# Kernel optimization log

Hardware: AMD Instinct MI355X
Metric: run time of the kernel (lower is better)

## Reference

```python
import jax, jax.numpy as jnp
import numpy as np

B, VH, VL, EP = 4, 130, 120, 256
DIN, DEP, D, H, NL = 256, 128, 512, 16, 8
HID = 4 * D

def _pe(x, base=1000.0):
    # sinusoidal positional encoding (base=1000 as in the module)
    L, Dm = x.shape[-2], x.shape[-1]
    pos = jnp.arange(L, dtype=jnp.float32)
    ch = jnp.arange(Dm, dtype=jnp.float32)
    ang = pos[:, None] / (base ** (2.0 * ch / ch[-1]))[None]
    enc = jnp.where(ch % 2 == 0, jnp.sin(ang), jnp.cos(ang))
    return x + enc

def _ln(x, g, b):
    m = x.mean(-1, keepdims=True)
    v = ((x - m) ** 2).mean(-1, keepdims=True)
    return (x - m) / jnp.sqrt(v + 1e-5) * g + b

def _gmha(x, rots, trans, mask_bias, qkv_w, out_w, out_b, g, b, r_s, d_s):
    # ESM3 geometric multi-head attention (algorithm 6)
    xn = _ln(x, g, b)
    qkv = (xn @ qkv_w.T).reshape(x.shape[0], x.shape[1], 5, H, 3)  # [B,L,5,H,3]
    qkv = jnp.einsum('brid,brfhd->brfhi', rots, qkv)               # rotate into global frame
    Qr, Kr, Qd, Kd, V = (qkv[..., f, :, :] for f in range(5))
    scale = 3.0 ** -0.5
    Ar = jnp.einsum('bihd,bjhd->bijh', Qr, Kr) * jax.nn.softplus(r_s) * scale
    qd = Qd + trans[:, :, None, :]
    kd = Kd + trans[:, :, None, :]
    dist = jnp.linalg.norm(qd[:, :, None] - kd[:, None], axis=-1)  # [B,i,j,H]
    logits = Ar - dist * jax.nn.softplus(d_s) * scale + mask_bias[..., None]
    A = jax.nn.softmax(logits, axis=2)
    o = jnp.einsum('bijh,bjhd->bihd', A, V)
    o = jnp.einsum('brji,brhj->brhi', rots, o)                     # rotate back (R^T)
    return o.reshape(x.shape[0], x.shape[1], H * 3) @ out_w.T + out_b

def _swiglu(x, g, b, w12, w3):
    # SwiGLU transition (dropout is identity in eval)
    h = _ln(x, g, b) @ w12.T
    a, v = jnp.split(h, 2, axis=-1)
    return (jax.nn.silu(a) * v) @ w3.T

def _forward(vh_x, vl_x, vh_rots, vh_trans, vl_rots, vl_trans, ep_feats, ep_rots, ep_trans,
             vh_emb_w, vl_emb_w, tgt_emb_w, qkv_w, out_w, out_b, ln_g, ln_b, r_scale, d_scale,
             ln2_g, ln2_b, w12, w3, out_vh_w, out_vh_gate_w, out_vh_gate_b,
             out_vl_w, out_vl_gate_w, out_vl_gate_b, vh_mask, vl_mask, ep_mask):
    emb = jnp.concatenate([_pe(vh_x @ vh_emb_w.T), _pe(vl_x @ vl_emb_w.T), ep_feats @ tgt_emb_w.T], axis=1)
    rots = jnp.concatenate([vh_rots, vl_rots, ep_rots], axis=1)
    trans = jnp.concatenate([vh_trans, vl_trans, ep_trans], axis=1)
    mask = jnp.concatenate([vh_mask, vl_mask, ep_mask], axis=1)
    mask_bias = jnp.where(mask[:, :, None] | mask[:, None, :], -1e9, 0.0)
    for i in range(NL):
        emb = emb + _gmha(emb, rots, trans, mask_bias, qkv_w[i], out_w[i], out_b[i],
                          ln_g[i], ln_b[i], r_scale[i], d_scale[i])
        emb = emb + _swiglu(emb, ln2_g[i], ln2_b[i], w12[i], w3[i])
    vh_e, vl_e = emb[:, :VH], emb[:, VH:VH + VL]
    vh_upd = (vh_e @ out_vh_w.T) * jax.nn.sigmoid(vh_e @ out_vh_gate_w.T + out_vh_gate_b)
    vl_upd = (vl_e @ out_vl_w.T) * jax.nn.sigmoid(vl_e @ out_vl_gate_w.T + out_vl_gate_b)
    vh_out = jnp.where(~vh_mask[..., None], vh_x + vh_upd, vh_x)
    vl_out = jnp.where(~vl_mask[..., None], vl_x + vl_upd, vl_x)
    return vh_out, vl_out

def setup_inputs():
    key = jax.random.key(0)
    ks = iter(jax.random.split(key, 40))
    s = 0.02
    return dict(
        vh_x=jax.random.normal(next(ks), (B, VH, DIN)),
        vl_x=jax.random.normal(next(ks), (B, VL, DIN)),
        vh_rots=jax.random.normal(next(ks), (B, VH, 3, 3)),
        vh_trans=jax.random.normal(next(ks), (B, VH, 3)),
        vl_rots=jax.random.normal(next(ks), (B, VL, 3, 3)),
        vl_trans=jax.random.normal(next(ks), (B, VL, 3)),
        ep_feats=jax.random.normal(next(ks), (B, EP, DEP)),
        ep_rots=jax.random.normal(next(ks), (B, EP, 3, 3)),
        ep_trans=jax.random.normal(next(ks), (B, EP, 3)),
        vh_mask=jnp.zeros((B, VH), dtype=bool),
        vl_mask=jnp.zeros((B, VL), dtype=bool),
        ep_mask=jax.random.randint(next(ks), (B, EP), 0, 2).astype(bool),
        vh_emb_w=jax.random.normal(next(ks), (D, DIN)) * s,
        vl_emb_w=jax.random.normal(next(ks), (D, DIN)) * s,
        tgt_emb_w=jax.random.normal(next(ks), (D, DEP)) * s,
        qkv_w=jax.random.normal(next(ks), (NL, H * 15, D)) * s,
        out_w=jax.random.normal(next(ks), (NL, D, H * 3)) * s,
        out_b=jnp.zeros((NL, D)),
        ln_g=jnp.ones((NL, D)), ln_b=jnp.zeros((NL, D)),
        r_scale=jnp.zeros((NL, H)), d_scale=jnp.zeros((NL, H)),
        ln2_g=jnp.ones((NL, D)), ln2_b=jnp.zeros((NL, D)),
        w12=jax.random.normal(next(ks), (NL, 2 * HID, D)) * s,
        w3=jax.random.normal(next(ks), (NL, D, HID)) * s,
        out_vh_w=jax.random.normal(next(ks), (DIN, D)) * s,
        out_vh_gate_w=jax.random.normal(next(ks), (DIN, D)) * s,
        out_vh_gate_b=jnp.full((DIN,), -2.0),
        out_vl_w=jax.random.normal(next(ks), (DIN, D)) * s,
        out_vl_gate_w=jax.random.normal(next(ks), (DIN, D)) * s,
        out_vl_gate_b=jnp.full((DIN,), -2.0),
    )

def reference(vh_x, vl_x, vh_rots, vh_trans, vl_rots, vl_trans, ep_feats, ep_rots, ep_trans,
              vh_mask, vl_mask, ep_mask,
              vh_emb_w, vl_emb_w, tgt_emb_w, qkv_w, out_w, out_b, ln_g, ln_b, r_scale, d_scale,
              ln2_g, ln2_b, w12, w3, out_vh_w, out_vh_gate_w, out_vh_gate_b,
              out_vl_w, out_vl_gate_w, out_vl_gate_b):
    return _forward(vh_x, vl_x, vh_rots, vh_trans, vl_rots, vl_trans, ep_feats, ep_rots, ep_trans,
                    vh_emb_w, vl_emb_w, tgt_emb_w, qkv_w, out_w, out_b, ln_g, ln_b, r_scale, d_scale,
                    ln2_g, ln2_b, w12, w3, out_vh_w, out_vh_gate_w, out_vh_gate_b,
                    out_vl_w, out_vl_gate_w, out_vl_gate_b, vh_mask, vl_mask, ep_mask)
```

## Files before the change

### kernel.cpp

```cpp
#include <hip/hip_runtime.h>
#include <hip/hip_bf16.h>
#include <math.h>
#include <stdint.h>

#define B_ 4
#define VH_ 130
#define VL_ 120
#define EP_ 256
#define R_ 506
#define RP_ 512
#define DIN_ 256
#define DEP_ 128
#define D_ 512
#define H_ 16
#define NL_ 8
#define HID_ 2048

#define MODE_STORE 0
#define MODE_ADD_BIAS 1

typedef _Float16 half8 __attribute__((ext_vector_type(8)));
typedef float f32x4 __attribute__((ext_vector_type(4)));

#define ASYNC16(ldsdst, gsrc)                                                  \
  __builtin_amdgcn_global_load_lds(                                            \
      (const __attribute__((address_space(1))) unsigned int*)(gsrc),           \
      (__attribute__((address_space(3))) unsigned int*)(ldsdst), 16, 0, 0)

__global__ __launch_bounds__(256) void gemm16sw_kernel(
    const _Float16* __restrict__ A, const _Float16* __restrict__ Wa,
    const _Float16* __restrict__ Wv, _Float16* __restrict__ Gh,
    int M, int K) {
  __shared__ _Float16 Al[4][4096];
  __shared__ _Float16 Ba[4][2048];
  __shared__ _Float16 Bv[4][2048];

  const int t = threadIdx.x;
  const int nbm = (M + 127) >> 7;
  const int nwg = gridDim.x;
  int bid = blockIdx.x;
  if ((nwg & 7) == 0) {
    int q = nwg >> 3;
    bid = (bid & 7) * q + (bid >> 3);
  }
  const int bm = bid % nbm, bn = bid / nbm;
  const int lane = t & 63;
  const int w = t >> 6;
  const int wm = w >> 1, wn = w & 1;

  const int r0 = t >> 2;
  const int cp = t & 3;
  const int gc = cp ^ ((r0 >> 1) & 3);
  int gr0 = bm * 128 + r0;       if (gr0 >= M) gr0 = M - 1;
  int gr1 = bm * 128 + 64 + r0;  if (gr1 >= M) gr1 = M - 1;
  const int gcol = bn * 64 + r0;
  const _Float16* pA0 = A + (size_t)gr0 * K + gc * 8;
  const _Float16* pA1 = A + (size_t)gr1 * K + gc * 8;
  const _Float16* pBa = Wa + (size_t)gcol * K + gc * 8;
  const _Float16* pBv = Wv + (size_t)gcol * K + gc * 8;

#define STAGE(buf, kt)                                                         \
  do {                                                                         \
    ASYNC16(&Al[buf][t * 8], pA0 + (size_t)(kt) * 32);                         \
    ASYNC16(&Al[buf][2048 + t * 8], pA1 + (size_t)(kt) * 32);                  \
    ASYNC16(&Ba[buf][t * 8], pBa + (size_t)(kt) * 32);                         \
    ASYNC16(&Bv[buf][t * 8], pBv + (size_t)(kt) * 32);                         \
  } while (0)

  f32x4 aca[4][2], acv[4][2];
#pragma unroll
  for (int i = 0; i < 4; i++)
#pragma unroll
    for (int j = 0; j < 2; j++) {
      aca[i][j] = (f32x4){0.f, 0.f, 0.f, 0.f};
      acv[i][j] = (f32x4){0.f, 0.f, 0.f, 0.f};
    }

  const int nt = K >> 5;
  STAGE(0, 0); STAGE(1, 1); STAGE(2, 2);

  const int rl = lane & 15;
  const int ca = (lane >> 4) ^ ((rl >> 1) & 3);
  for (int kt = 0; kt < nt; ++kt) {
    if (kt < nt - 2)       asm volatile("s_waitcnt vmcnt(8)" ::: "memory");
    else if (kt == nt - 2) asm volatile("s_waitcnt vmcnt(4)" ::: "memory");
    else                   asm volatile("s_waitcnt vmcnt(0)" ::: "memory");
    __builtin_amdgcn_s_barrier();
    const int buf = kt & 3;
    const _Float16* Ab  = &Al[buf][(wm * 64 + rl) * 32 + ca * 8];
    const _Float16* Bab = &Ba[buf][(wn * 32 + rl) * 32 + ca * 8];
    const _Float16* Bvb = &Bv[buf][(wn * 32 + rl) * 32 + ca * 8];
    half8 af[4], bfa[2], bfv[2];
#pragma unroll
    for (int i = 0; i < 4; i++) af[i] = *(const half8*)(Ab + i * 512);
#pragma unroll
    for (int j = 0; j < 2; j++) {
      bfa[j] = *(const half8*)(Bab + j * 512);
      bfv[j] = *(const half8*)(Bvb + j * 512);
    }
#pragma unroll
    for (int i = 0; i < 4; i++)
#pragma unroll
      for (int j = 0; j < 2; j++) {
        aca[i][j] = __builtin_amdgcn_mfma_f32_16x16x32_f16(af[i], bfa[j],
                                                           aca[i][j], 0, 0, 0);
        acv[i][j] = __builtin_amdgcn_mfma_f32_16x16x32_f16(af[i], bfv[j],
                                                           acv[i][j], 0, 0, 0);
      }
    if (kt + 3 < nt) STAGE((kt + 3) & 3, kt + 3);
  }
#undef STAGE

  const int rb = bm * 128 + wm * 64 + ((lane >> 4) << 2);
  const int cb = bn * 64 + wn * 32 + (lane & 15);
#pragma unroll
  for (int i = 0; i < 4; i++) {
#pragma unroll
    for (int j = 0; j < 2; j++) {
      int col = cb + j * 16;
#pragma unroll
      for (int q = 0; q < 4; q++) {
        int row = rb + i * 16 + q;
        if (row >= M) continue;
        float a = aca[i][j][q];
        float v = acv[i][j][q];
        Gh[(size_t)row * HID_ + col] = (_Float16)((a / (1.f + expf(-a))) * v);
      }
    }
  }
}

__global__ __launch_bounds__(256) void gemm16b_kernel(
    const _Float16* __restrict__ A, const _Float16* __restrict__ W,
    float* __restrict__ C, const float* __restrict__ bias,
    int M, int N, int K, int mode, int crpb, int cR, int cbase, int pe) {
  __shared__ _Float16 Al[4][2048];
  __shared__ _Float16 Bl[4][2048];

  const int t = threadIdx.x;
  const int nbm = (M + 63) >> 6;
  const int nwg = gridDim.x;
  int bid = blockIdx.x;
  if ((nwg & 7) == 0) {
    int q = nwg >> 3;
    bid = (bid & 7) * q + (bid >> 3);
  }
  const int bm = bid % nbm, bn = bid / nbm;
  const int lane = t & 63;
  const int w = t >> 6;
  const int wm = w >> 1, wn = w & 1;

  const int r0 = t >> 2;
  const int cp = t & 3;
  const int gc = cp ^ ((r0 >> 1) & 3);
  int gr = bm * 64 + r0;    if (gr >= M) gr = M - 1;
  int gcol = bn * 64 + r0;  if (gcol >= N) gcol = N - 1;
  const _Float16* pA = A + (size_t)gr * K + gc * 8;
  const _Float16* pB = W + (size_t)gcol * K + gc * 8;

#define STAGE(buf, kt)                                                         \
  do {                                                                         \
    ASYNC16(&Al[buf][t * 8], pA + (size_t)(kt) * 32);                          \
    ASYNC16(&Bl[buf][t * 8], pB + (size_t)(kt) * 32);                          \
  } while (0)

  f32x4 acc[2][2];
#pragma unroll
  for (int i = 0; i < 2; i++)
#pragma unroll
    for (int j = 0; j < 2; j++) acc[i][j] = (f32x4){0.f, 0.f, 0.f, 0.f};

  const int nt = K >> 5;
  STAGE(0, 0); STAGE(1, 1); STAGE(2, 2);

  const int rl = lane & 15;
  const int ca = (lane >> 4) ^ ((rl >> 1) & 3);
  for (int kt = 0; kt < nt; ++kt) {
    if (kt < nt - 2)       asm volatile("s_waitcnt vmcnt(4)" ::: "memory");
    else if (kt == nt - 2) asm volatile("s_waitcnt vmcnt(2)" ::: "memory");
    else                   asm volatile("s_waitcnt vmcnt(0)" ::: "memory");
    __builtin_amdgcn_s_barrier();
    const int buf = kt & 3;
    half8 af[2], bf[2];
#pragma unroll
    for (int i = 0; i < 2; i++)
      af[i] = *(const half8*)&Al[buf][(wm * 32 + i * 16 + rl) * 32 + ca * 8];
#pragma unroll
    for (int j = 0; j < 2; j++)
      bf[j] = *(const half8*)&Bl[buf][(wn * 32 + j * 16 + rl) * 32 + ca * 8];
#pragma unroll
    for (int i = 0; i < 2; i++)
#pragma unroll
      for (int j = 0; j < 2; j++)
        acc[i][j] = __builtin_amdgcn_mfma_f32_16x16x32_f16(af[i], bf[j],
                                                           acc[i][j], 0, 0, 0);
    if (kt + 3 < nt) STAGE((kt + 3) & 3, kt + 3);
  }
#undef STAGE

  const float PEK = -0.02703623196464017f;
  const int rb = bm * 64 + wm * 32 + ((lane >> 4) << 2);
  const int cb = bn * 64 + wn * 32 + (lane & 15);
#pragma unroll
  for (int i = 0; i < 2; i++) {
#pragma unroll
    for (int j = 0; j < 2; j++) {
      int col = cb + j * 16;
      if (col >= N) continue;
#pragma unroll
      for (int q = 0; q < 4; q++) {
        int row = rb + i * 16 + q;
        if (row >= M) continue;
        int crow = (row / crpb) * cR + cbase + row % crpb;
        size_t idx = (size_t)crow * N + col;
        float v = acc[i][j][q];
        if (pe) {
          float pos = (float)(row % crpb);
          float ang = pos * expf((float)col * PEK);
          v += (col & 1) ? cosf(ang) : sinf(ang);
        }
        if (mode == MODE_STORE) C[idx] = v;
        else {
          float bb = bias ? bias[col] : 0.f;
          C[idx] = C[idx] + v + bb;
        }
      }
    }
  }
}

__global__ __launch_bounds__(256) void gemm16gate_kernel(
    const _Float16* __restrict__ A, const _Float16* __restrict__ Wv,
    const _Float16* __restrict__ Wg, const float* __restrict__ x,
    const float* __restrict__ gb, const int* __restrict__ mask,
    float* __restrict__ out, int M, int K, int arpb, int aR, int abase) {
  __shared__ _Float16 Al[4][2048];
  __shared__ _Float16 Bva[4][2048];
  __shared__ _Float16 Bga[4][2048];

  const int t = threadIdx.x;
  const int nbm = (M + 63) >> 6;
  const int nwg = gridDim.x;
  int bid = blockIdx.x;
  if ((nwg & 7) == 0) {
    int q = nwg >> 3;
    bid = (bid & 7) * q + (bid >> 3);
  }
  const int bm = bid % nbm, bn = bid / nbm;
  const int lane = t & 63;
  const int w = t >> 6;
  const int wm = w >> 1, wn = w & 1;

  const int r0 = t >> 2;
  const int cp = t & 3;
  const int gc = cp ^ ((r0 >> 1) & 3);
  int gr = bm * 64 + r0;  if (gr >= M) gr = M - 1;
  int ar = (gr / arpb) * aR + abase + gr % arpb;
  const int gcol = bn * 64 + r0;
  const _Float16* pA  = A + (size_t)ar * K + gc * 8;
  const _Float16* pBv = Wv + (size_t)gcol * K + gc * 8;
  const _Float16* pBg = Wg + (size_t)gcol * K + gc * 8;

#define STAGE(buf, kt)                                                         \
  do {                                                                         \
    ASYNC16(&Al[buf][t * 8], pA + (size_t)(kt) * 32);                          \
    ASYNC16(&Bva[buf][t * 8], pBv + (size_t)(kt) * 32);                        \
    ASYNC16(&Bga[buf][t * 8], pBg + (size_t)(kt) * 32);                        \
  } while (0)

  f32x4 acv[2][2], acg[2][2];
#pragma unroll
  for (int i = 0; i < 2; i++)
#pragma unroll
    for (int j = 0; j < 2; j++) {
      acv[i][j] = (f32x4){0.f, 0.f, 0.f, 0.f};
      acg[i][j] = (f32x4){0.f, 0.f, 0.f, 0.f};
    }

  const int nt = K >> 5;
  STAGE(0, 0); STAGE(1, 1); STAGE(2, 2);

  const int rl = lane & 15;
  const int ca = (lane >> 4) ^ ((rl >> 1) & 3);
  for (int kt = 0; kt < nt; ++kt) {
    if (kt < nt - 2)       asm volatile("s_waitcnt vmcnt(6)" ::: "memory");
    else if (kt == nt - 2) asm volatile("s_waitcnt vmcnt(3)" ::: "memory");
    else                   asm volatile("s_waitcnt vmcnt(0)" ::: "memory");
    __builtin_amdgcn_s_barrier();
    const int buf = kt & 3;
    half8 af[2], bv[2], bg2[2];
#pragma unroll
    for (int i = 0; i < 2; i++)
      af[i] = *(const half8*)&Al[buf][(wm * 32 + i * 16 + rl) * 32 + ca * 8];
#pragma unroll
    for (int j = 0; j < 2; j++) {
      bv[j] = *(const half8*)&Bva[buf][(wn * 32 + j * 16 + rl) * 32 + ca * 8];
      bg2[j] = *(const half8*)&Bga[buf][(wn * 32 + j * 16 + rl) * 32 + ca * 8];
    }
#pragma unroll
    for (int i = 0; i < 2; i++)
#pragma unroll
      for (int j = 0; j < 2; j++) {
        acv[i][j] = __builtin_amdgcn_mfma_f32_16x16x32_f16(af[i], bv[j],
                                                           acv[i][j], 0, 0, 0);
        acg[i][j] = __builtin_amdgcn_mfma_f32_16x16x32_f16(af[i], bg2[j],
                                                           acg[i][j], 0, 0, 0);
      }
    if (kt + 3 < nt) STAGE((kt + 3) & 3, kt + 3);
  }
#undef STAGE

  const int rb = bm * 64 + wm * 32 + ((lane >> 4) << 2);
  const int cb = bn * 64 + wn * 32 + (lane & 15);
#pragma unroll
  for (int i = 0; i < 2; i++) {
#pragma unroll
    for (int j = 0; j < 2; j++) {
      int col = cb + j * 16;
#pragma unroll
      for (int q = 0; q < 4; q++) {
        int row = rb + i * 16 + q;
        if (row >= M) continue;
        size_t idx = (size_t)row * DIN_ + col;
        float xv = x[idx];
        float res;
        if (mask[row]) {
          res = xv;
        } else {
          float gate = 1.f / (1.f + expf(-(acg[i][j][q] + gb[col])));
          res = xv + acv[i][j][q] * gate;
        }
        out[idx] = res;
      }
    }
  }
}

__global__ __launch_bounds__(256) void ln_kernel(
    const float* __restrict__ x, const float* __restrict__ g,
    const float* __restrict__ b, _Float16* __restrict__ out) {
  const int row = blockIdx.x;
  const int t = threadIdx.x;
  const float* xr = x + (size_t)row * D_;
  float v0 = xr[t], v1 = xr[t + 256];
  float s = v0 + v1, s2 = v0 * v0 + v1 * v1;
#pragma unroll
  for (int o = 32; o > 0; o >>= 1) {
    s += __shfl_down(s, o);
    s2 += __shfl_down(s2, o);
  }
  __shared__ float w1[4], w2[4], mv[2];
  const int w = t >> 6;
  if ((t & 63) == 0) { w1[w] = s; w2[w] = s2; }
  __syncthreads();
  if (t == 0) {
    float ss = w1[0] + w1[1] + w1[2] + w1[3];
    float ss2 = w2[0] + w2[1] + w2[2] + w2[3];
    float mean = ss * (1.f / D_);
    float var = ss2 * (1.f / D_) - mean * mean;
    mv[0] = mean;
    mv[1] = rsqrtf(var + 1e-5f);
  }
  __syncthreads();
  float mean = mv[0], inv = mv[1];
  _Float16* orow = out + (size_t)row * D_;
  orow[t] = (_Float16)((v0 - mean) * inv * g[t] + b[t]);
  orow[t + 256] = (_Float16)((v1 - mean) * inv * g[t + 256] + b[t + 256]);
}

struct ThSegs {
  const float* src[13];
  _Float16* dst[13];
  int cum[14];
};
__global__ void tohalf_multi_kernel(ThSegs sg) {
  int total = sg.cum[13];
  for (int i = blockIdx.x * blockDim.x + threadIdx.x; i < total;
       i += gridDim.x * blockDim.x) {
    int s = 0;
    while (i >= sg.cum[s + 1]) s++;
    int off = i - sg.cum[s];
    const float4* p = (const float4*)(sg.src[s] + (size_t)off * 16);
    float4 x = p[0], y = p[1], z = p[2], w = p[3];
    half8 h0 = {(_Float16)x.x, (_Float16)x.y, (_Float16)x.z, (_Float16)x.w,
                (_Float16)y.x, (_Float16)y.y, (_Float16)y.z, (_Float16)y.w};
    half8 h1 = {(_Float16)z.x, (_Float16)z.y, (_Float16)z.z, (_Float16)z.w,
                (_Float16)w.x, (_Float16)w.y, (_Float16)w.z, (_Float16)w.w};
    half8* d = (half8*)(sg.dst[s] + (size_t)off * 16);
    d[0] = h0;
    d[1] = h1;
  }
}

__global__ void tohalf_kernel(const float* __restrict__ src,
                              _Float16* __restrict__ dst, int n8) {
  for (int i = blockIdx.x * blockDim.x + threadIdx.x; i < n8;
       i += gridDim.x * blockDim.x) {
    const float4* s = (const float4*)(src + (size_t)i * 8);
    float4 x = s[0], y = s[1];
    half8 h = {(_Float16)x.x, (_Float16)x.y, (_Float16)x.z, (_Float16)x.w,
               (_Float16)y.x, (_Float16)y.y, (_Float16)y.z, (_Float16)y.w};
    *(half8*)(dst + (size_t)i * 8) = h;
  }
}

__global__ void transpose_ow_kernel(const float* __restrict__ out_w,
                                    float* __restrict__ owT) {
  int idx = blockIdx.x * blockDim.x + threadIdx.x;
  const int total = NL_ * 48 * D_;
  if (idx >= total) return;
  int l = idx / (48 * D_);
  int rem = idx % (48 * D_);
  int k = rem / D_;
  int c = rem % D_;
  owT[idx] = out_w[(size_t)l * D_ * 48 + (size_t)c * 48 + k];
}

__global__ void prep_kernel(
    const float* __restrict__ vh_rots, const float* __restrict__ vh_trans,
    const float* __restrict__ vl_rots, const float* __restrict__ vl_trans,
    const float* __restrict__ ep_rots, const float* __restrict__ ep_trans,
    const int* __restrict__ vh_mask, const int* __restrict__ vl_mask,
    const int* __restrict__ ep_mask, float* __restrict__ rots,
    float* __restrict__ trans, int* __restrict__ mask,
    int* __restrict__ maskp, float* __restrict__ Kt, float* __restrict__ PKt,
    float* __restrict__ Vt) {
  int idx = blockIdx.x * blockDim.x + threadIdx.x;
  if (idx < B_ * RP_) {
    int b = idx >> 9, r = idx & (RP_ - 1);
    if (r >= R_) {
      maskp[idx] = 1;
      return;
    }
    const float* sr; const float* st; int sm;
    if (r < VH_) {
      sr = vh_rots + (size_t)(b * VH_ + r) * 9;
      st = vh_trans + (size_t)(b * VH_ + r) * 3;
      sm = vh_mask[b * VH_ + r];
    } else if (r < VH_ + VL_) {
      int rr = r - VH_;
      sr = vl_rots + (size_t)(b * VL_ + rr) * 9;
      st = vl_trans + (size_t)(b * VL_ + rr) * 3;
      sm = vl_mask[b * VL_ + rr];
    } else {
      int rr = r - VH_ - VL_;
      sr = ep_rots + (size_t)(b * EP_ + rr) * 9;
      st = ep_trans + (size_t)(b * EP_ + rr) * 3;
      sm = ep_mask[b * EP_ + rr];
    }
    int lin = b * R_ + r;
    maskp[idx] = sm;
    mask[lin] = sm;
#pragma unroll
    for (int k = 0; k < 9; k++) rots[(size_t)lin * 9 + k] = sr[k];
#pragma unroll
    for (int k = 0; k < 3; k++) trans[(size_t)lin * 3 + k] = st[k];
  } else {
    int p = idx - B_ * RP_;
    const int per = B_ * H_ * 3 * (RP_ - R_);
    if (p >= 3 * per) return;
    int a = p / per;
    int q = p % per;
    int chan = q / (RP_ - R_), jj = q % (RP_ - R_);
    float* dst = (a == 0) ? Kt : (a == 1) ? PKt : Vt;
    dst[(size_t)chan * RP_ + R_ + jj] = 0.f;
  }
}

__global__ __launch_bounds__(128) void rotate_kernel(
    const float* __restrict__ qkv_raw, const float* __restrict__ rots,
    const float* __restrict__ trans, float* __restrict__ Qrow,
    float* __restrict__ PQrow, float* __restrict__ Kt,
    float* __restrict__ PKt, float* __restrict__ Vt) {
  const int blk = blockIdx.x;
  const int b = blk / R_;
  const int r = blk % R_;
  const int t = threadIdx.x;
  __shared__ float Rm[9], tr[3], raw[240];
  if (t < 9) Rm[t] = rots[(size_t)blk * 9 + t];
  if (t >= 9 && t < 12) tr[t - 9] = trans[(size_t)blk * 3 + (t - 9)];
  for (int i = t; i < 240; i += 128) raw[i] = qkv_raw[(size_t)blk * 240 + i];
  __syncthreads();
  if (t < 80) {
    int f = t / 16, h = t % 16;
    float x = raw[f * 48 + h * 3 + 0];
    float y = raw[f * 48 + h * 3 + 1];
    float z = raw[f * 48 + h * 3 + 2];
    float r0 = Rm[0] * x + Rm[1] * y + Rm[2] * z;
    float r1 = Rm[3] * x + Rm[4] * y + Rm[5] * z;
    float r2 = Rm[6] * x + Rm[7] * y + Rm[8] * z;
    if (f == 2 || f == 3) { r0 += tr[0]; r1 += tr[1]; r2 += tr[2]; }
    if (f == 0 || f == 2) {
      float* dst = (f == 0) ? Qrow : PQrow;
      size_t o = (size_t)blk * 48 + h * 3;
      dst[o] = r0; dst[o + 1] = r1; dst[o + 2] = r2;
    } else {
      float* dst = (f == 1) ? Kt : (f == 3) ? PKt : Vt;
      size_t base = ((size_t)(b * H_ + h) * 3) * RP_ + r;
      dst[base] = r0; dst[base + RP_] = r1; dst[base + 2 * RP_] = r2;
    }
  }
}

__global__ __launch_bounds__(1024) void attn2_kernel(
    const float* __restrict__ Qrow, const float* __restrict__ PQrow,
    const float* __restrict__ Kt, const float* __restrict__ PKt,
    const float* __restrict__ Vt, const float* __restrict__ rots,
    const int* __restrict__ mask, const int* __restrict__ maskp,
    const float* __restrict__ rs, const float* __restrict__ ds,
    const float* __restrict__ owT, const float* __restrict__ out_b,
    float* __restrict__ emb) {
  const int blk = blockIdx.x;
  const int b = blk / (R_ / 2);
  const int ip = blk % (R_ / 2);
  const int i0 = ip * 2;
  const int t = threadIdx.x;
  const int lane = t & 63;
  const int h = t >> 6;

  __shared__ float qs[2][48], ps[2][48], og[2][48];
  __shared__ float crs[16], cds[16];
  __shared__ int mi[2];

  if (t < 96) {
    int io = t / 48, k2 = t % 48;
    int i = i0 + io;
    qs[io][k2] = Qrow[((size_t)(b * R_ + i)) * 48 + k2];
    ps[io][k2] = PQrow[((size_t)(b * R_ + i)) * 48 + k2];
  } else if (t < 112) {
    int hh = t - 96;
    const float sc = 0.57735026918962576f;
    crs[hh] = log1pf(expf(rs[hh])) * sc;
    cds[hh] = log1pf(expf(ds[hh])) * sc;
  } else if (t < 114) {
    mi[t - 112] = mask[b * R_ + i0 + (t - 112)];
  }
  __syncthreads();

  float mb[8];
#pragma unroll
  for (int jb = 0; jb < 8; jb++) {
    int j = jb * 64 + lane;
    mb[jb] = maskp[b * RP_ + j] ? -1e9f : 0.f;
  }
  const float bi0 = mi[0] ? -1e9f : 0.f;
  const float bi1 = mi[1] ? -1e9f : 0.f;

  {
    const float sA = crs[h], sD = cds[h];
    const float qx0 = qs[0][h * 3], qy0 = qs[0][h * 3 + 1], qz0 = qs[0][h * 3 + 2];
    const float px0 = ps[0][h * 3], py0 = ps[0][h * 3 + 1], pz0 = ps[0][h * 3 + 2];
    const float qx1 = qs[1][h * 3], qy1 = qs[1][h * 3 + 1], qz1 = qs[1][h * 3 + 2];
    const float px1 = ps[1][h * 3], py1 = ps[1][h * 3 + 1], pz1 = ps[1][h * 3 + 2];
    const float* kb = Kt + ((size_t)(b * H_ + h) * 3) * RP_;
    const float* pb = PKt + ((size_t)(b * H_ + h) * 3) * RP_;
    const float* vb = Vt + ((size_t)(b * H_ + h) * 3) * RP_;

    float l0[8], l1[8];
    float m0 = -3e38f, m1 = -3e38f;
#pragma unroll
    for (int jb = 0; jb < 8; jb++) {
      int j = jb * 64 + lane;
      float kx = kb[j], ky = kb[j + RP_], kz = kb[j + 2 * RP_];
      float pkx = pb[j], pky = pb[j + RP_], pkz = pb[j + 2 * RP_];
      float dx0 = px0 - pkx, dy0 = py0 - pky, dz0 = pz0 - pkz;
      float d0 = sqrtf(dx0 * dx0 + dy0 * dy0 + dz0 * dz0);
      l0[jb] = (qx0 * kx + qy0 * ky + qz0 * kz) * sA - d0 * sD + mb[jb] + bi0;
      m0 = fmaxf(m0, l0[jb]);
      float dx1 = px1 - pkx, dy1 = py1 - pky, dz1 = pz1 - pkz;
      float d1 = sqrtf(dx1 * dx1 + dy1 * dy1 + dz1 * dz1);
      l1[jb] = (qx1 * kx + qy1 * ky + qz1 * kz) * sA - d1 * sD + mb[jb] + bi1;
      m1 = fmaxf(m1, l1[jb]);
    }
#pragma unroll
    for (int s = 1; s < 64; s <<= 1) {
      m0 = fmaxf(m0, __shfl_xor(m0, s));
      m1 = fmaxf(m1, __shfl_xor(m1, s));
    }
    float s0 = 0.f, s1 = 0.f;
    float ox0 = 0.f, oy0 = 0.f, oz0 = 0.f, ox1 = 0.f, oy1 = 0.f, oz1 = 0.f;
#pragma unroll
    for (int jb = 0; jb < 8; jb++) {
      int j = jb * 64 + lane;
      float p0 = expf(l0[jb] - m0);
      float p1 = expf(l1[jb] - m1);
      s0 += p0; s1 += p1;
      float vx = vb[j], vy = vb[j + RP_], vz = vb[j + 2 * RP_];
      ox0 += p0 * vx; oy0 += p0 * vy; oz0 += p0 * vz;
      ox1 += p1 * vx; oy1 += p1 * vy; oz1 += p1 * vz;
    }
#pragma unroll
    for (int s = 1; s < 64; s <<= 1) {
      s0 += __shfl_xor(s0, s); s1 += __shfl_xor(s1, s);
      ox0 += __shfl_xor(ox0, s); oy0 += __shfl_xor(oy0, s); oz0 += __shfl_xor(oz0, s);
      ox1 += __shfl_xor(ox1, s); oy1 += __shfl_xor(oy1, s); oz1 += __shfl_xor(oz1, s);
    }
    if (lane == 0) {
      og[0][h * 3] = ox0 / s0; og[0][h * 3 + 1] = oy0 / s0; og[0][h * 3 + 2] = oz0 / s0;
      og[1][h * 3] = ox1 / s1; og[1][h * 3 + 1] = oy1 / s1; og[1][h * 3 + 2] = oz1 / s1;
    }
  }
  __syncthreads();
  float r0v0 = 0.f, r0v1 = 0.f;
  if (t < 48) {
    int hh = t / 3, i3 = t % 3;
    const float* Rm0 = rots + ((size_t)(b * R_ + i0)) * 9;
    const float* Rm1 = rots + ((size_t)(b * R_ + i0 + 1)) * 9;
    r0v0 = Rm0[0 + i3] * og[0][hh * 3 + 0] + Rm0[3 + i3] * og[0][hh * 3 + 1] +
           Rm0[6 + i3] * og[0][hh * 3 + 2];
    r0v1 = Rm1[0 + i3] * og[1][hh * 3 + 0] + Rm1[3 + i3] * og[1][hh * 3 + 1] +
           Rm1[6 + i3] * og[1][hh * 3 + 2];
  }
  __syncthreads();
  if (t < 48) { og[0][t] = r0v0; og[1][t] = r0v1; }
  __syncthreads();
  {
    const int io = t >> 9;
    const int c = t & 511;
    float* erow = emb + ((size_t)(b * R_ + i0 + io)) * D_;
    float a0 = 0.f, a1 = 0.f, a2 = 0.f, a3 = 0.f;
#pragma unroll
    for (int k = 0; k < 48; k += 4) {
      a0 += og[io][k + 0] * owT[(size_t)(k + 0) * D_ + c];
      a1 += og[io][k + 1] * owT[(size_t)(k + 1) * D_ + c];
      a2 += og[io][k + 2] * owT[(size_t)(k + 2) * D_ + c];
      a3 += og[io][k + 3] * owT[(size_t)(k + 3) * D_ + c];
    }
    erow[c] += out_b[c] + ((a0 + a1) + (a2 + a3));
  }
}

extern "C" void kernel_launch(void* const* d_in, const int* in_sizes, int n_in,
                              void* d_out, int out_size, void* d_ws, size_t ws_size,
                              hipStream_t stream) {
  const float* vh_x = (const float*)d_in[0];
  const float* vl_x = (const float*)d_in[1];
  const float* vh_rots = (const float*)d_in[2];
  const float* vh_trans = (const float*)d_in[3];
  const float* vl_rots = (const float*)d_in[4];
  const float* vl_trans = (const float*)d_in[5];
  const float* ep_feats = (const float*)d_in[6];
  const float* ep_rots = (const float*)d_in[7];
  const float* ep_trans = (const float*)d_in[8];
  const int* vh_mask = (const int*)d_in[9];
  const int* vl_mask = (const int*)d_in[10];
  const int* ep_mask = (const int*)d_in[11];
  const float* vh_emb_w = (const float*)d_in[12];
  const float* vl_emb_w = (const float*)d_in[13];
  const float* tgt_emb_w = (const float*)d_in[14];
  const float* qkv_w = (const float*)d_in[15];
  const float* out_w = (const float*)d_in[16];
  const float* out_b = (const float*)d_in[17];
  const float* ln_g = (const float*)d_in[18];
  const float* ln_b = (const float*)d_in[19];
  const float* r_scale = (const float*)d_in[20];
  const float* d_scale = (const float*)d_in[21];
  const float* ln2_g = (const float*)d_in[22];
  const float* ln2_b = (const float*)d_in[23];
  const float* w12 = (const float*)d_in[24];
  const float* w3 = (const float*)d_in[25];
  const float* out_vh_w = (const float*)d_in[26];
  const float* out_vh_gate_w = (const float*)d_in[27];
  const float* out_vh_gate_b = (const float*)d_in[28];
  const float* out_vl_w = (const float*)d_in[29];
  const float* out_vl_gate_w = (const float*)d_in[30];
  const float* out_vl_gate_b = (const float*)d_in[31];

  const int BR = B_ * R_;

  uint8_t* P = (uint8_t*)d_ws;
  auto alloc = [&](size_t bytes) {
    uint8_t* p = P;
    P += (bytes + 255) & ~(size_t)255;
    return p;
  };
  float* emb = (float*)alloc((size_t)BR * D_ * 4);
  _Float16* xnh = (_Float16*)alloc((size_t)BR * D_ * 2);
  float* qkvr = (float*)alloc((size_t)BR * 240 * 4);
  float* Qrow = (float*)alloc((size_t)BR * 48 * 4);
  float* PQrow = (float*)alloc((size_t)BR * 48 * 4);
  float* Kt = (float*)alloc((size_t)B_ * H_ * 3 * RP_ * 4);
  float* PKt = (float*)alloc((size_t)B_ * H_ * 3 * RP_ * 4);
  float* Vt = (float*)alloc((size_t)B_ * H_ * 3 * RP_ * 4);
  _Float16* ghalf = (_Float16*)alloc((size_t)BR * HID_ * 2);
  float* rots_c = (float*)alloc((size_t)BR * 9 * 4);
  float* trans_c = (float*)alloc((size_t)BR * 3 * 4);
  int* mask_c = (int*)alloc((size_t)BR * 4);
  int* maskp = (int*)alloc((size_t)B_ * RP_ * 4);
  float* owT = (float*)alloc((size_t)NL_ * 48 * D_ * 4);
  _Float16* embh = (_Float16*)alloc((size_t)BR * D_ * 2);
  _Float16* qkvh = (_Float16*)alloc((size_t)NL_ * 240 * D_ * 2);
  _Float16* w12h = (_Float16*)alloc((size_t)NL_ * 2 * HID_ * D_ * 2);
  _Float16* w3h = (_Float16*)alloc((size_t)NL_ * D_ * HID_ * 2);
  _Float16* vhxh = (_Float16*)alloc((size_t)B_ * VH_ * DIN_ * 2);
  _Float16* vlxh = (_Float16*)alloc((size_t)B_ * VL_ * DIN_ * 2);
  _Float16* eph = (_Float16*)alloc((size_t)B_ * EP_ * DEP_ * 2);
  _Float16* vhewh = (_Float16*)alloc((size_t)D_ * DIN_ * 2);
  _Float16* vlewh = (_Float16*)alloc((size_t)D_ * DIN_ * 2);
  _Float16* tgewh = (_Float16*)alloc((size_t)D_ * DEP_ * 2);
  _Float16* ovhw = (_Float16*)alloc((size_t)DIN_ * D_ * 2);
  _Float16* ovhgw = (_Float16*)alloc((size_t)DIN_ * D_ * 2);
  _Float16* ovlw = (_Float16*)alloc((size_t)DIN_ * D_ * 2);
  _Float16* ovlgw = (_Float16*)alloc((size_t)DIN_ * D_ * 2);

  {
    ThSegs sg;
    const float* srcs[13] = {qkv_w, w12, w3, vh_x, vl_x, ep_feats,
                             vh_emb_w, vl_emb_w, tgt_emb_w,
                             out_vh_w, out_vh_gate_w, out_vl_w, out_vl_gate_w};
    _Float16* dsts[13] = {qkvh, w12h, w3h, vhxh, vlxh, eph,
                          vhewh, vlewh, tgewh, ovhw, ovhgw, ovlw, ovlgw};
    int n16s[13] = {NL_ * 240 * D_ / 16, NL_ * 2 * HID_ * D_ / 16,
                    NL_ * D_ * HID_ / 16, B_ * VH_ * DIN_ / 16,
                    B_ * VL_ * DIN_ / 16, B_ * EP_ * DEP_ / 16,
                    D_ * DIN_ / 16, D_ * DIN_ / 16, D_ * DEP_ / 16,
                    DIN_ * D_ / 16, DIN_ * D_ / 16, DIN_ * D_ / 16,
                    DIN_ * D_ / 16};
    int c = 0;
    for (int i = 0; i < 13; i++) {
      sg.src[i] = srcs[i]; sg.dst[i] = dsts[i];
      sg.cum[i] = c; c += n16s[i];
    }
    sg.cum[13] = c;
    tohalf_multi_kernel<<<2048, 256, 0, stream>>>(sg);
  }

  {
    int total = NL_ * 48 * D_;
    transpose_ow_kernel<<<(total + 255) / 256, 256, 0, stream>>>(out_w, owT);
  }

  {
    int total = B_ * RP_ + 3 * B_ * H_ * 3 * (RP_ - R_);
    prep_kernel<<<(total + 255) / 256, 256, 0, stream>>>(
        vh_rots, vh_trans, vl_rots, vl_trans, ep_rots, ep_trans, vh_mask,
        vl_mask, ep_mask, rots_c, trans_c, mask_c, maskp, Kt, PKt, Vt);
  }

  auto gemm16b = [&](const _Float16* A, const _Float16* W, float* C,
                     const float* bias, int M, int N, int K, int mode,
                     int crpb, int cR, int cbase, int pe) {
    int nbm = (M + 63) / 64, nbn = (N + 63) / 64;
    gemm16b_kernel<<<nbm * nbn, 256, 0, stream>>>(A, W, C, bias, M, N, K, mode,
                                                  crpb, cR, cbase, pe);
  };

  gemm16b(vhxh, vhewh, emb, nullptr, B_ * VH_, D_, DIN_, MODE_STORE,
          VH_, R_, 0, 1);
  gemm16b(vlxh, vlewh, emb, nullptr, B_ * VL_, D_, DIN_, MODE_STORE,
          VL_, R_, VH_, 1);
  gemm16b(eph, tgewh, emb, nullptr, B_ * EP_, D_, DEP_, MODE_STORE,
          EP_, R_, VH_ + VL_, 0);

  for (int l = 0; l < NL_; l++) {
    const _Float16* qwh = qkvh + (size_t)l * 240 * D_;
    const float* owTl = owT + (size_t)l * 48 * D_;
    const float* obias = out_b + (size_t)l * D_;
    const float* lg = ln_g + (size_t)l * D_;
    const float* lb = ln_b + (size_t)l * D_;
    const float* l2g = ln2_g + (size_t)l * D_;
    const float* l2b = ln2_b + (size_t)l * D_;
    const float* rs = r_scale + (size_t)l * H_;
    const float* dsc = d_scale + (size_t)l * H_;
    const _Float16* w12ah = w12h + (size_t)l * 2 * HID_ * D_;
    const _Float16* w12bh = w12ah + (size_t)HID_ * D_;
    const _Float16* w3lh = w3h + (size_t)l * D_ * HID_;

    ln_kernel<<<BR, 256, 0, stream>>>(emb, lg, lb, xnh);
    gemm16b(xnh, qwh, qkvr, nullptr, BR, 240, D_, MODE_STORE, BR, BR, 0, 0);
    rotate_kernel<<<BR, 128, 0, stream>>>(qkvr, rots_c, trans_c, Qrow, PQrow,
                                          Kt, PKt, Vt);
    attn2_kernel<<<B_ * (R_ / 2), 1024, 0, stream>>>(
        Qrow, PQrow, Kt, PKt, Vt, rots_c, mask_c, maskp, rs, dsc, owTl, obias,
        emb);

    ln_kernel<<<BR, 256, 0, stream>>>(emb, l2g, l2b, xnh);
    {
      int nbm = (BR + 127) / 128, nbn = HID_ / 64;
      gemm16sw_kernel<<<nbm * nbn, 256, 0, stream>>>(xnh, w12ah, w12bh, ghalf,
                                                     BR, D_);
    }
    gemm16b(ghalf, w3lh, emb, nullptr, BR, D_, HID_, MODE_ADD_BIAS,
            BR, BR, 0, 0);
  }

  tohalf_kernel<<<1024, 256, 0, stream>>>(emb, embh, BR * D_ / 8);
  {
    int M = B_ * VH_;
    int nbm = (M + 63) / 64;
    gemm16gate_kernel<<<nbm * 4, 256, 0, stream>>>(
        embh, ovhw, ovhgw, vh_x, out_vh_gate_b, vh_mask, (float*)d_out, M, D_,
        VH_, R_, 0);
  }
  {
    int M = B_ * VL_;
    int nbm = (M + 63) / 64;
    gemm16gate_kernel<<<nbm * 4, 256, 0, stream>>>(
        embh, ovlw, ovlgw, vl_x, out_vl_gate_b, vl_mask,
        (float*)d_out + (size_t)B_ * VH_ * DIN_, M, D_, VL_, R_, VH_);
  }
}
```

Baseline: 1.200 ms.

## Pack K/PK/V as padded float4 rows and shrink attention blocks to 256 threads

Changes the K, PK and V buffers from three separate channel planes to an interleaved float4-per-row layout padded with a zero fourth lane. Each attention lane now fetches a key or value with one 16-byte vector load instead of three strided scalar loads. The attention kernel drops from 1024 to 256 threads, with each wave looping over four heads and each thread computing two output columns in the projection. This aims to cut load instructions and block size, at the cost of a third more memory traffic from the padding and less parallelism per block.

```diff
diff --git a/kernel.cpp b/kernel.cpp
--- a/kernel.cpp
+++ b/kernel.cpp
@@ -457,13 +457,14 @@
     for (int k = 0; k < 3; k++) trans[(size_t)lin * 3 + k] = st[k];
   } else {
     int p = idx - B_ * RP_;
-    const int per = B_ * H_ * 3 * (RP_ - R_);
+    const int per = B_ * H_ * (RP_ - R_) * 4;
     if (p >= 3 * per) return;
     int a = p / per;
     int q = p % per;
-    int chan = q / (RP_ - R_), jj = q % (RP_ - R_);
+    int bh = q / ((RP_ - R_) * 4);
+    int rem = q % ((RP_ - R_) * 4);
     float* dst = (a == 0) ? Kt : (a == 1) ? PKt : Vt;
-    dst[(size_t)chan * RP_ + R_ + jj] = 0.f;
+    dst[(size_t)bh * RP_ * 4 + (size_t)R_ * 4 + rem] = 0.f;
   }
 }
 
@@ -496,13 +497,13 @@
       dst[o] = r0; dst[o + 1] = r1; dst[o + 2] = r2;
     } else {
       float* dst = (f == 1) ? Kt : (f == 3) ? PKt : Vt;
-      size_t base = ((size_t)(b * H_ + h) * 3) * RP_ + r;
-      dst[base] = r0; dst[base + RP_] = r1; dst[base + 2 * RP_] = r2;
-    }
-  }
-}
-
-__global__ __launch_bounds__(1024) void attn2_kernel(
+      size_t base = ((size_t)(b * H_ + h) * RP_ + r) * 4;
+      *(float4*)(dst + base) = make_float4(r0, r1, r2, 0.f);
+    }
+  }
+}
+
+__global__ __launch_bounds__(256) void attn2_kernel(
     const float* __restrict__ Qrow, const float* __restrict__ PQrow,
     const float* __restrict__ Kt, const float* __restrict__ PKt,
     const float* __restrict__ Vt, const float* __restrict__ rots,
@@ -516,7 +517,7 @@
   const int i0 = ip * 2;
   const int t = threadIdx.x;
   const int lane = t & 63;
-  const int h = t >> 6;
+  const int w = t >> 6;
 
   __shared__ float qs[2][48], ps[2][48], og[2][48];
   __shared__ float crs[16], cds[16];
@@ -528,10 +529,10 @@
     qs[io][k2] = Qrow[((size_t)(b * R_ + i)) * 48 + k2];
     ps[io][k2] = PQrow[((size_t)(b * R_ + i)) * 48 + k2];
   } else if (t < 112) {
-    int hh = t - 96;
+    int h = t - 96;
     const float sc = 0.57735026918962576f;
-    crs[hh] = log1pf(expf(rs[hh])) * sc;
-    cds[hh] = log1pf(expf(ds[hh])) * sc;
+    crs[h] = log1pf(expf(rs[h])) * sc;
+    cds[h] = log1pf(expf(ds[h])) * sc;
   } else if (t < 114) {
     mi[t - 112] = mask[b * R_ + i0 + (t - 112)];
   }
@@ -546,30 +547,31 @@
   const float bi0 = mi[0] ? -1e9f : 0.f;
   const float bi1 = mi[1] ? -1e9f : 0.f;
 
-  {
+  for (int hh = 0; hh < 4; hh++) {
+    const int h = hh * 4 + w;
     const float sA = crs[h], sD = cds[h];
     const float qx0 = qs[0][h * 3], qy0 = qs[0][h * 3 + 1], qz0 = qs[0][h * 3 + 2];
     const float px0 = ps[0][h * 3], py0 = ps[0][h * 3 + 1], pz0 = ps[0][h * 3 + 2];
     const float qx1 = qs[1][h * 3], qy1 = qs[1][h * 3 + 1], qz1 = qs[1][h * 3 + 2];
     const float px1 = ps[1][h * 3], py1 = ps[1][h * 3 + 1], pz1 = ps[1][h * 3 + 2];
-    const float* kb = Kt + ((size_t)(b * H_ + h) * 3) * RP_;
-    const float* pb = PKt + ((size_t)(b * H_ + h) * 3) * RP_;
-    const float* vb = Vt + ((size_t)(b * H_ + h) * 3) * RP_;
+    const float4* kb4 = (const float4*)(Kt + ((size_t)(b * H_ + h) * RP_) * 4);
+    const float4* pb4 = (const float4*)(PKt + ((size_t)(b * H_ + h) * RP_) * 4);
+    const float4* vb4 = (const float4*)(Vt + ((size_t)(b * H_ + h) * RP_) * 4);
 
     float l0[8], l1[8];
     float m0 = -3e38f, m1 = -3e38f;
 #pragma unroll
     for (int jb = 0; jb < 8; jb++) {
       int j = jb * 64 + lane;
-      float kx = kb[j], ky = kb[j + RP_], kz = kb[j + 2 * RP_];
-      float pkx = pb[j], pky = pb[j + RP_], pkz = pb[j + 2 * RP_];
-      float dx0 = px0 - pkx, dy0 = py0 - pky, dz0 = pz0 - pkz;
+      float4 k4 = kb4[j];
+      float4 p4 = pb4[j];
+      float dx0 = px0 - p4.x, dy0 = py0 - p4.y, dz0 = pz0 - p4.z;
       float d0 = sqrtf(dx0 * dx0 + dy0 * dy0 + dz0 * dz0);
-      l0[jb] = (qx0 * kx + qy0 * ky + qz0 * kz) * sA - d0 * sD + mb[jb] + bi0;
+      l0[jb] = (qx0 * k4.x + qy0 * k4.y + qz0 * k4.z) * sA - d0 * sD + mb[jb] + bi0;
       m0 = fmaxf(m0, l0[jb]);
-      float dx1 = px1 - pkx, dy1 = py1 - pky, dz1 = pz1 - pkz;
+      float dx1 = px1 - p4.x, dy1 = py1 - p4.y, dz1 = pz1 - p4.z;
       float d1 = sqrtf(dx1 * dx1 + dy1 * dy1 + dz1 * dz1);
-      l1[jb] = (qx1 * kx + qy1 * ky + qz1 * kz) * sA - d1 * sD + mb[jb] + bi1;
+      l1[jb] = (qx1 * k4.x + qy1 * k4.y + qz1 * k4.z) * sA - d1 * sD + mb[jb] + bi1;
       m1 = fmaxf(m1, l1[jb]);
     }
 #pragma unroll
@@ -585,9 +587,9 @@
       float p0 = expf(l0[jb] - m0);
       float p1 = expf(l1[jb] - m1);
       s0 += p0; s1 += p1;
-      float vx = vb[j], vy = vb[j + RP_], vz = vb[j + 2 * RP_];
-      ox0 += p0 * vx; oy0 += p0 * vy; oz0 += p0 * vz;
-      ox1 += p1 * vx; oy1 += p1 * vy; oz1 += p1 * vz;
+      float4 v4 = vb4[j];
+      ox0 += p0 * v4.x; oy0 += p0 * v4.y; oz0 += p0 * v4.z;
+      ox1 += p1 * v4.x; oy1 += p1 * v4.y; oz1 += p1 * v4.z;
     }
 #pragma unroll
     for (int s = 1; s < 64; s <<= 1) {
@@ -614,19 +616,22 @@
   __syncthreads();
   if (t < 48) { og[0][t] = r0v0; og[1][t] = r0v1; }
   __syncthreads();
-  {
-    const int io = t >> 9;
-    const int c = t & 511;
+#pragma unroll
+  for (int io = 0; io < 2; io++) {
     float* erow = emb + ((size_t)(b * R_ + i0 + io)) * D_;
-    float a0 = 0.f, a1 = 0.f, a2 = 0.f, a3 = 0.f;
-#pragma unroll
-    for (int k = 0; k < 48; k += 4) {
-      a0 += og[io][k + 0] * owT[(size_t)(k + 0) * D_ + c];
-      a1 += og[io][k + 1] * owT[(size_t)(k + 1) * D_ + c];
-      a2 += og[io][k + 2] * owT[(size_t)(k + 2) * D_ + c];
-      a3 += og[io][k + 3] * owT[(size_t)(k + 3) * D_ + c];
-    }
-    erow[c] += out_b[c] + ((a0 + a1) + (a2 + a3));
+#pragma unroll
+    for (int half = 0; half < 2; half++) {
+      int c = half * 256 + t;
+      float a0 = 0.f, a1 = 0.f, a2 = 0.f, a3 = 0.f;
+#pragma unroll
+      for (int k = 0; k < 48; k += 4) {
+        a0 += og[io][k + 0] * owT[(size_t)(k + 0) * D_ + c];
+        a1 += og[io][k + 1] * owT[(size_t)(k + 1) * D_ + c];
+        a2 += og[io][k + 2] * owT[(size_t)(k + 2) * D_ + c];
+        a3 += og[io][k + 3] * owT[(size_t)(k + 3) * D_ + c];
+      }
+      erow[c] += out_b[c] + ((a0 + a1) + (a2 + a3));
+    }
   }
 }
 
@@ -679,9 +684,9 @@
   float* qkvr = (float*)alloc((size_t)BR * 240 * 4);
   float* Qrow = (float*)alloc((size_t)BR * 48 * 4);
   float* PQrow = (float*)alloc((size_t)BR * 48 * 4);
-  float* Kt = (float*)alloc((size_t)B_ * H_ * 3 * RP_ * 4);
-  float* PKt = (float*)alloc((size_t)B_ * H_ * 3 * RP_ * 4);
-  float* Vt = (float*)alloc((size_t)B_ * H_ * 3 * RP_ * 4);
+  float* Kt = (float*)alloc((size_t)B_ * H_ * RP_ * 4 * 4);
+  float* PKt = (float*)alloc((size_t)B_ * H_ * RP_ * 4 * 4);
+  float* Vt = (float*)alloc((size_t)B_ * H_ * RP_ * 4 * 4);
   _Float16* ghalf = (_Float16*)alloc((size_t)BR * HID_ * 2);
   float* rots_c = (float*)alloc((size_t)BR * 9 * 4);
   float* trans_c = (float*)alloc((size_t)BR * 3 * 4);
@@ -731,7 +736,7 @@
   }
 
   {
-    int total = B_ * RP_ + 3 * B_ * H_ * 3 * (RP_ - R_);
+    int total = B_ * RP_ + 3 * B_ * H_ * (RP_ - R_) * 4;
     prep_kernel<<<(total + 255) / 256, 256, 0, stream>>>(
         vh_rots, vh_trans, vl_rots, vl_trans, ep_rots, ep_trans, vh_mask,
         vl_mask, ep_mask, rots_c, trans_c, mask_c, maskp, Kt, PKt, Vt);
@@ -770,7 +775,7 @@
     gemm16b(xnh, qwh, qkvr, nullptr, BR, 240, D_, MODE_STORE, BR, BR, 0, 0);
     rotate_kernel<<<BR, 128, 0, stream>>>(qkvr, rots_c, trans_c, Qrow, PQrow,
                                           Kt, PKt, Vt);
-    attn2_kernel<<<B_ * (R_ / 2), 1024, 0, stream>>>(
+    attn2_kernel<<<B_ * (R_ / 2), 256, 0, stream>>>(
         Qrow, PQrow, Kt, PKt, Vt, rots_c, mask_c, maskp, rs, dsc, owTl, obias,
         emb);
 
```

Result: faster. 1.083 ms (-9.8%).
